# Kernel optimization log

Measured on AMD Instinct MI355X. Metric: run time of the kernel, lower is better.

The kernel has to match this reference:

```python
import jax, jax.numpy as jnp
import numpy as np

EMBED = 1024
HEADS = 16
HEAD_DIM = EMBED // HEADS
DIVIDER = int(np.sqrt(HEAD_DIM))  # torch code uses int(sqrt(head_dim)) == 8


def setup_inputs() -> dict:
    key = jax.random.key(0)
    ks = jax.random.split(key, 9)
    B, S = 2, 2048
    scale = 1.0 / np.sqrt(EMBED)
    def lin(kw, kb):
        W = jax.random.uniform(kw, (EMBED, EMBED), jnp.float32, -scale, scale)
        b = jax.random.uniform(kb, (EMBED,), jnp.float32, -scale, scale)
        return W, b
    Wq, bq = lin(ks[0], ks[1])
    Wk, bk = lin(ks[2], ks[3])
    Wv, bv = lin(ks[4], ks[5])
    Wo, bo = lin(ks[6], ks[7])
    x = jax.random.normal(ks[8], (B, S, EMBED), jnp.float32)
    return {"x": x, "Wq": Wq, "bq": bq, "Wk": Wk, "bk": bk,
            "Wv": Wv, "bv": bv, "Wo": Wo, "bo": bo}


def reference(x, Wq, bq, Wk, bk, Wv, bv, Wo, bo):
    B, S, _ = x.shape
    # projections (torch Linear: x @ W.T + b)
    q = x @ Wq.T + bq
    k = x @ Wk.T + bk
    v = x @ Wv.T + bv
    # split heads: [B, S, H, D] -> [B, H, S, D]
    def heads(t):
        return t.reshape(B, S, HEADS, HEAD_DIM).transpose(0, 2, 1, 3)
    q, k, v = heads(q), heads(k), heads(v)
    # scores [B, H, S, S]
    scores = jnp.einsum('bhsd,bhtd->bhst', q, k) / DIVIDER
    attn = jax.nn.softmax(scores, axis=-1)
    out = jnp.einsum('bhst,bhtd->bhsd', attn, v)
    out = out.transpose(0, 2, 1, 3).reshape(B, S, EMBED)
    return out @ Wo.T + bo
```

## Files before the change

kernel.cpp:

```cpp
#include <hip/hip_runtime.h>
#include <hip/hip_bf16.h>
#include <stdint.h>

using bf16 = __hip_bfloat16;
typedef __attribute__((ext_vector_type(8))) short   short8;
typedef __attribute__((ext_vector_type(4))) float   floatx4;
typedef __attribute__((ext_vector_type(2))) unsigned int uint2v;

static __device__ __forceinline__ unsigned short f2bf(float f) {
    return __builtin_bit_cast(unsigned short, __float2bfloat16(f));
}

static __device__ __forceinline__ uint4 load8bf(const void* p, size_t e, int f) {
    if (!f) return *(const uint4*)((const ushort*)p + e);
    const float* fp = (const float*)p + e;
    float4 a = *(const float4*)fp;
    float4 b = *(const float4*)(fp + 4);
    union { uint4 u; unsigned short s[8]; } r;
    r.s[0] = f2bf(a.x); r.s[1] = f2bf(a.y); r.s[2] = f2bf(a.z); r.s[3] = f2bf(a.w);
    r.s[4] = f2bf(b.x); r.s[5] = f2bf(b.y); r.s[6] = f2bf(b.z); r.s[7] = f2bf(b.w);
    return r.u;
}
static __device__ __forceinline__ float loadScalar(const void* p, int i, int f) {
    return f ? ((const float*)p)[i] : __bfloat162float(((const bf16*)p)[i]);
}

__global__ void detect_dtype(const ushort* __restrict__ x, int* __restrict__ flag) {
    __shared__ int cnt;
    if (threadIdx.x == 0) cnt = 0;
    __syncthreads();
    unsigned short u = x[threadIdx.x * 2];
    int e = (u >> 7) & 0xFF;
    int bad = (e > 133 || e < 94) ? 1 : 0;
    atomicAdd(&cnt, bad);
    __syncthreads();
    if (threadIdx.x == 0) *flag = (cnt > 64) ? 1 : 0;
}

template<int BM>
__global__ __launch_bounds__(512, 4)
void gemm_bt(const void* __restrict__ A,
             const void* __restrict__ Wa, const void* __restrict__ Wb,
             const void* __restrict__ Ba, const void* __restrict__ Bb,
             void* __restrict__ Oa, void* __restrict__ Ob_,
             int pa, int pb, int a_ext, int out_ext,
             const int* __restrict__ flagp)
{
    constexpr int MB = BM / 128;
    constexpr int P  = BM / 64;
    constexpr int SG = BM / 8;
    __shared__ ushort pool[BM * 64 + 4096];

    const int f  = *flagp;
    const int fA = a_ext ? f : 0;
    const int z  = blockIdx.z;
    const void* W   = z ? Wb : Wa;
    const void* Bi  = z ? Bb : Ba;
    void*       Out = z ? Ob_ : Oa;
    const int   pm  = z ? pb : pa;

    const int m0 = blockIdx.x * BM;
    const int n0 = blockIdx.y * 64;
    const int tid  = threadIdx.x;
    const int lane = tid & 63;
    const int wave = tid >> 6;
    const int r15  = lane & 15;
    const int quad = lane >> 4;

    const int srow = tid >> 3;
    const int sg   = tid & 7;

    ushort* xs  = pool;
    ushort* wsm = pool + BM * 64;

    floatx4 acc[MB][4];
#pragma unroll
    for (int mb = 0; mb < MB; mb++)
#pragma unroll
        for (int db = 0; db < 4; db++) acc[mb][db] = (floatx4){0.f, 0.f, 0.f, 0.f};

    uint4 apre[P], wpre;
#pragma unroll
    for (int p = 0; p < P; p++)
        apre[p] = load8bf(A, (size_t)(m0 + srow + p * 64) * 1024 + sg * 8, fA);
    wpre = load8bf(W, (size_t)(n0 + srow) * 1024 + sg * 8, f);

    for (int kb = 0; kb < 1024; kb += 64) {
#pragma unroll
        for (int p = 0; p < P; p++) {
            int row = srow + p * 64;
            *(uint4*)(&xs[row * 64 + ((sg ^ (row & 7)) << 3)]) = apre[p];
        }
        *(uint4*)(&wsm[srow * 64 + ((sg ^ (srow & 7)) << 3)]) = wpre;
        __syncthreads();
        if (kb + 64 < 1024) {
#pragma unroll
            for (int p = 0; p < P; p++)
                apre[p] = load8bf(A, (size_t)(m0 + srow + p * 64) * 1024
                                      + kb + 64 + sg * 8, fA);
            wpre = load8bf(W, (size_t)(n0 + srow) * 1024 + kb + 64 + sg * 8, f);
        }
#pragma unroll
        for (int ks = 0; ks < 2; ks++) {
            short8 af[MB];
#pragma unroll
            for (int mb = 0; mb < MB; mb++) {
                int arow = wave * (16 * MB) + mb * 16 + r15;
                af[mb] = *(const short8*)(
                    &xs[arow * 64 + (((ks * 4 + quad) ^ (arow & 7)) << 3)]);
            }
#pragma unroll
            for (int db = 0; db < 4; db++) {
                int brow = db * 16 + r15;
                short8 bv = *(const short8*)(
                    &wsm[brow * 64 + (((ks * 4 + quad) ^ (brow & 7)) << 3)]);
#pragma unroll
                for (int mb = 0; mb < MB; mb++)
                    acc[mb][db] = __builtin_amdgcn_mfma_f32_16x16x32_bf16(
                        af[mb], bv, acc[mb][db], 0, 0, 0);
            }
        }
        __syncthreads();
    }

    if (pm == 2) {
#pragma unroll
        for (int mb = 0; mb < MB; mb++)
#pragma unroll
            for (int db = 0; db < 4; db++) {
                int d = db * 16 + r15;
                float bias = loadScalar(Bi, n0 + d, f);
                int s4 = wave * (16 * MB) + mb * 16 + quad * 4;
                union { uint2 u; ushort us[4]; } pk;
#pragma unroll
                for (int r = 0; r < 4; r++) pk.us[r] = f2bf(acc[mb][db][r] + bias);
                *(uint2*)(&pool[d * BM + (((s4 >> 3) ^ (d & 15)) << 3) + (s4 & 7)])
                    = pk.u;
            }
        __syncthreads();
        const int b_  = m0 >> 11;
        const int h   = n0 >> 6;
        const int sl0 = m0 & 2047;
#pragma unroll
        for (int rr = 0; rr < (64 * SG) / 512; rr++) {
            int idx = rr * 512 + tid;
            int d = idx / SG, sgrp = idx % SG;
            uint4 v = *(const uint4*)(&pool[d * BM + ((sgrp ^ (d & 15)) << 3)]);
            *(uint4*)((ushort*)Out +
                      ((size_t)((b_ * 16 + h) * 64 + d) << 11) + sl0 + sgrp * 8) = v;
        }
        return;
    }

#pragma unroll
    for (int mb = 0; mb < MB; mb++)
#pragma unroll
        for (int db = 0; db < 4; db++) {
            int col = n0 + db * 16 + r15;
            float bias = loadScalar(Bi, col, f);
#pragma unroll
            for (int r = 0; r < 4; r++) {
                int row = m0 + wave * (16 * MB) + mb * 16 + quad * 4 + r;
                float v = acc[mb][db][r] + bias;
                if (pm == 1) {
                    int hh = col >> 6, d = col & 63;
                    int b_ = row >> 11, s = row & 2047;
                    ((ushort*)Out)[(((size_t)(b_ * 16 + hh) * 2048 + s) << 6) + d]
                        = f2bf(v);
                } else if (out_ext && f) {
                    ((float*)Out)[(size_t)row * 1024 + col] = v;
                } else {
                    ((ushort*)Out)[(size_t)row * 1024 + col] = f2bf(v);
                }
            }
        }
}

__global__ __launch_bounds__(512, 4)
void attn_fused(const void* __restrict__ x, const void* __restrict__ Wq,
                const void* __restrict__ bq,
                const ushort* __restrict__ K, const ushort* __restrict__ VT,
                ushort* __restrict__ AO, const int* __restrict__ flagp)
{
    __shared__ ushort pool[24576];

    const int f   = *flagp;
    const int bh  = blockIdx.x;
    const int h   = bh & 15, b_ = bh >> 4;
    const int q0  = blockIdx.y * 128;
    const int tid  = threadIdx.x;
    const int lane = tid & 63;
    const int wave = tid >> 6;
    const int qg   = wave >> 1;
    const int kh   = wave & 1;
    const int r15  = lane & 15;
    const int quad = lane >> 4;
    const size_t base = (size_t)bh << 17;

    const int srow = tid >> 3;
    const int sg   = tid & 7;

    uint4 kpre = *(const uint4*)(K  + base + (size_t)srow * 64   + sg * 8);
    uint4 vpre = *(const uint4*)(VT + base + (size_t)srow * 2048 + sg * 8);

    floatx4 qacc[4];
#pragma unroll
    for (int db = 0; db < 4; db++) qacc[db] = (floatx4){0.f,0.f,0.f,0.f};

    uint4 xpre[2], wpre;
#pragma unroll
    for (int p = 0; p < 2; p++)
        xpre[p] = load8bf(x, (size_t)(b_ * 2048 + q0 + srow + p * 64) * 1024
                              + sg * 8, f);
    wpre = load8bf(Wq, (size_t)(h * 64 + srow) * 1024 + sg * 8, f);

    for (int kb = 0; kb < 1024; kb += 64) {
        int buf = (kb >> 6) & 1;
        ushort* xs  = pool + buf * 8192;
        ushort* wsm = pool + 16384 + buf * 4096;
#pragma unroll
        for (int p = 0; p < 2; p++) {
            int row = srow + p * 64;
            *(uint4*)(&xs[row * 64 + ((sg ^ (row & 7)) << 3)]) = xpre[p];
        }
        *(uint4*)(&wsm[srow * 64 + ((sg ^ (srow & 7)) << 3)]) = wpre;
        __syncthreads();
        if (kb + 64 < 1024) {
#pragma unroll
            for (int p = 0; p < 2; p++)
                xpre[p] = load8bf(x, (size_t)(b_ * 2048 + q0 + srow + p * 64) * 1024
                                      + kb + 64 + sg * 8, f);
            wpre = load8bf(Wq, (size_t)(h * 64 + srow) * 1024 + kb + 64 + sg * 8, f);
        }
#pragma unroll
        for (int ks = 0; ks < 2; ks++) {
            int arow = wave * 16 + r15;
            short8 af = *(const short8*)(
                &xs[arow * 64 + (((ks * 4 + quad) ^ (arow & 7)) << 3)]);
#pragma unroll
            for (int db = 0; db < 4; db++) {
                int brow = db * 16 + r15;
                short8 bv = *(const short8*)(
                    &wsm[brow * 64 + (((ks * 4 + quad) ^ (brow & 7)) << 3)]);
                qacc[db] = __builtin_amdgcn_mfma_f32_16x16x32_bf16(
                    af, bv, qacc[db], 0, 0, 0);
            }
        }
    }

    ushort* Qs = pool;
    const float csc = 0.1803368801f;
#pragma unroll
    for (int db = 0; db < 4; db++) {
        int d = db * 16 + r15;
        float bias = loadScalar(bq, h * 64 + d, f);
#pragma unroll
        for (int r = 0; r < 4; r++) {
            int q = wave * 16 + quad * 4 + r;
            Qs[q * 64 + (((d >> 3) ^ (q & 7)) << 3) + (d & 7)] =
                f2bf((qacc[db][r] + bias) * csc);
        }
    }
    __syncthreads();
    short8 qf2[2][2];
#pragma unroll
    for (int qb = 0; qb < 2; qb++)
#pragma unroll
        for (int ks = 0; ks < 2; ks++) {
            int arow = qg * 32 + qb * 16 + r15;
            qf2[qb][ks] = *(const short8*)(
                &Qs[arow * 64 + (((ks * 4 + quad) ^ (arow & 7)) << 3)]);
        }
    __syncthreads();

    floatx4 oacc[2][4], lacc[2];
#pragma unroll
    for (int qb = 0; qb < 2; qb++) {
#pragma unroll
        for (int db = 0; db < 4; db++) oacc[qb][db] = (floatx4){0.f,0.f,0.f,0.f};
        lacc[qb] = (floatx4){0.f,0.f,0.f,0.f};
    }
    short8 ones;
#pragma unroll
    for (int j = 0; j < 8; j++) ones[j] = (short)0x3F80;

    for (int t0 = 0; t0 < 2048; t0 += 64) {
        int buf = (t0 >> 6) & 1;
        ushort* Ks = pool + buf * 4096;
        ushort* Vt = pool + 8192 + buf * 4096;
        *(uint4*)(&Ks[srow * 64 + ((sg ^ (srow & 7)) << 3)]) = kpre;
        *(uint4*)(&Vt[srow * 64 + ((sg ^ (srow & 7)) << 3)]) = vpre;
        __syncthreads();
        if (t0 < 1984) {
            kpre = *(const uint4*)(K  + base + (size_t)(t0 + 64 + srow) * 64
                                       + sg * 8);
            vpre = *(const uint4*)(VT + base + (size_t)srow * 2048
                                       + t0 + 64 + sg * 8);
        }

        floatx4 s[2][2];
#pragma unroll
        for (int mb = 0; mb < 2; mb++)
#pragma unroll
            for (int qb = 0; qb < 2; qb++) s[mb][qb] = (floatx4){0.f,0.f,0.f,0.f};
#pragma unroll
        for (int ks = 0; ks < 2; ks++)
#pragma unroll
            for (int mb = 0; mb < 2; mb++) {
                int arow = kh * 32 + mb * 16 + r15;
                short8 kf = *(const short8*)(
                    &Ks[arow * 64 + (((ks * 4 + quad) ^ (arow & 7)) << 3)]);
#pragma unroll
                for (int qb = 0; qb < 2; qb++)
                    s[mb][qb] = __builtin_amdgcn_mfma_f32_16x16x32_bf16(
                        kf, qf2[qb][ks], s[mb][qb], 0, 0, 0);
            }

        uint Lr[2][2], Hr[2][2];
#pragma unroll
        for (int mb = 0; mb < 2; mb++)
#pragma unroll
            for (int qb = 0; qb < 2; qb++) {
                uint b0 = __builtin_bit_cast(uint, __builtin_amdgcn_exp2f(s[mb][qb][0]));
                uint b1 = __builtin_bit_cast(uint, __builtin_amdgcn_exp2f(s[mb][qb][1]));
                uint b2 = __builtin_bit_cast(uint, __builtin_amdgcn_exp2f(s[mb][qb][2]));
                uint b3 = __builtin_bit_cast(uint, __builtin_amdgcn_exp2f(s[mb][qb][3]));
                Lr[mb][qb] = (b1 & 0xFFFF0000u) | (b0 >> 16);
                Hr[mb][qb] = (b3 & 0xFFFF0000u) | (b2 >> 16);
            }
        short8 pf[2];
#pragma unroll
        for (int qb = 0; qb < 2; qb++) {
            uint2v tL = __builtin_amdgcn_permlane32_swap(
                Lr[0][qb], Lr[1][qb], false, false);
            uint2v uL = __builtin_amdgcn_permlane16_swap(
                tL[0], tL[1], false, false);
            uint2v tH = __builtin_amdgcn_permlane32_swap(
                Hr[0][qb], Hr[1][qb], false, false);
            uint2v uH = __builtin_amdgcn_permlane16_swap(
                tH[0], tH[1], false, false);
            union { uint u[4]; short8 s8; } pk;
            pk.u[0] = uL[0]; pk.u[1] = uH[0]; pk.u[2] = uL[1]; pk.u[3] = uH[1];
            pf[qb] = pk.s8;
        }

#pragma unroll
        for (int db = 0; db < 4; db++) {
            int brow = db * 16 + r15;
            short8 vf = *(const short8*)(
                &Vt[brow * 64 + (((kh * 4 + quad) ^ (brow & 7)) << 3)]);
#pragma unroll
            for (int qb = 0; qb < 2; qb++)
                oacc[qb][db] = __builtin_amdgcn_mfma_f32_16x16x32_bf16(
                    pf[qb], vf, oacc[qb][db], 0, 0, 0);
        }
#pragma unroll
        for (int qb = 0; qb < 2; qb++)
            lacc[qb] = __builtin_amdgcn_mfma_f32_16x16x32_bf16(
                pf[qb], ones, lacc[qb], 0, 0, 0);
    }

    __syncthreads();
    {
        char* rb = (char*)pool + qg * 10240 + lane * 16;
        if (kh) {
#pragma unroll
            for (int qb = 0; qb < 2; qb++) {
#pragma unroll
                for (int db = 0; db < 4; db++)
                    *(floatx4*)(rb + (qb * 4 + db) * 1024) = oacc[qb][db];
                *(floatx4*)(rb + (8 + qb) * 1024) = lacc[qb];
            }
        }
        __syncthreads();
        if (!kh) {
#pragma unroll
            for (int qb = 0; qb < 2; qb++) {
#pragma unroll
                for (int db = 0; db < 4; db++)
                    oacc[qb][db] += *(const floatx4*)(rb + (qb * 4 + db) * 1024);
                lacc[qb] += *(const floatx4*)(rb + (8 + qb) * 1024);
            }
            float inv[2][4];
#pragma unroll
            for (int qb = 0; qb < 2; qb++)
#pragma unroll
                for (int r = 0; r < 4; r++) inv[qb][r] = 1.f / lacc[qb][r];
#pragma unroll
            for (int qb = 0; qb < 2; qb++)
#pragma unroll
                for (int db = 0; db < 4; db++) {
                    int d = db * 16 + r15;
#pragma unroll
                    for (int r = 0; r < 4; r++) {
                        int qi = q0 + qg * 32 + qb * 16 + quad * 4 + r;
                        AO[((size_t)(b_ * 2048 + qi) << 10) + h * 64 + d] =
                            f2bf(oacc[qb][db][r] * inv[qb][r]);
                    }
                }
        }
    }
}

__global__ void copy_u4(const uint4* __restrict__ src, uint4* __restrict__ dst) {
    size_t i = (size_t)blockIdx.x * 256 + threadIdx.x;
    dst[i] = src[i];
}

extern "C" void kernel_launch(void* const* d_in, const int* in_sizes, int n_in,
                              void* d_out, int out_size, void* d_ws, size_t ws_size,
                              hipStream_t stream)
{
    const void* x  = d_in[0];
    const void* Wq = d_in[1];
    const void* bq = d_in[2];
    const void* Wk = d_in[3];
    const void* bk = d_in[4];
    const void* Wv = d_in[5];
    const void* bv = d_in[6];
    const void* Wo = d_in[7];
    const void* bo = d_in[8];

    const size_t TEN = (size_t)2 * 16 * 2048 * 64;
    int*    flagp = (int*)d_ws;
    ushort* Kw    = (ushort*)((char*)d_ws + 256);
    ushort* Vw    = Kw + TEN;
    const bool big_ws = ws_size >= 3 * TEN * sizeof(ushort) + 256;
    ushort* AOw   = big_ws ? (Vw + TEN) : (ushort*)d_out;
    ushort* Oin   = big_ws ? AOw : Kw;

    detect_dtype<<<1, 256, 0, stream>>>((const ushort*)x, flagp);

    gemm_bt<128><<<dim3(32, 16, 2), dim3(512), 0, stream>>>(
        x, Wk, Wv, bk, bv, Kw, Vw, 1, 2, 1,
        0, flagp);

    attn_fused<<<dim3(32, 16), dim3(512), 0, stream>>>(
        x, Wq, bq, Kw, Vw, AOw, flagp);

    if (!big_ws)
        copy_u4<<<dim3(2048), dim3(256), 0, stream>>>(
            (const uint4*)d_out, (uint4*)Oin);

    gemm_bt<128><<<dim3(32, 16, 1), dim3(512), 0, stream>>>(
        Oin, Wo, Wo, bo, bo, d_out, d_out, 0, 0, 0,
        1, flagp);
}
```

Measured before the change: 224.1 us.

## Pre-convert inputs to bf16 and use direct global-to-LDS loads in GEMMs

```diff
diff --git a/kernel.cpp b/kernel.cpp
--- a/kernel.cpp
+++ b/kernel.cpp
@@ -24,6 +24,11 @@
 static __device__ __forceinline__ float loadScalar(const void* p, int i, int f) {
     return f ? ((const float*)p)[i] : __bfloat162float(((const bf16*)p)[i]);
 }
+
+#define GLL16(g, l)                                                          \
+    __builtin_amdgcn_global_load_lds(                                        \
+        (const __attribute__((address_space(1))) void*)(g),                  \
+        (__attribute__((address_space(3))) void*)(l), 16, 0, 0)
 
 __global__ void detect_dtype(const ushort* __restrict__ x, int* __restrict__ flag) {
     __shared__ int cnt;
@@ -35,6 +40,136 @@
     atomicAdd(&cnt, bad);
     __syncthreads();
     if (threadIdx.x == 0) *flag = (cnt > 64) ? 1 : 0;
+}
+
+__global__ void cvt_bf16(const void* __restrict__ x,  const void* __restrict__ Wq,
+                         const void* __restrict__ Wk, const void* __restrict__ Wv,
+                         const void* __restrict__ Wo,
+                         ushort* __restrict__ out, const int* __restrict__ flagp)
+{
+    const int f = *flagp;
+    const size_t M1 = (size_t)1 << 20, M4 = (size_t)4 << 20;
+    size_t i = ((size_t)blockIdx.x * 256 + threadIdx.x) * 8;
+    const void* src; size_t off;
+    if (i < M4)            { src = x;  off = i; }
+    else if (i < M4 + M1)  { src = Wq; off = i - M4; }
+    else if (i < M4 + 2*M1){ src = Wk; off = i - (M4 + M1); }
+    else if (i < M4 + 3*M1){ src = Wv; off = i - (M4 + 2*M1); }
+    else                   { src = Wo; off = i - (M4 + 3*M1); }
+    *(uint4*)(out + i) = load8bf(src, off, f);
+}
+
+__global__ __launch_bounds__(512, 4)
+void gemm_lds(const ushort* __restrict__ A,
+              const ushort* __restrict__ Wa, const ushort* __restrict__ Wb2,
+              const void* __restrict__ Ba, const void* __restrict__ Bb,
+              void* __restrict__ Oa, void* __restrict__ Ob_,
+              int pa, int pb, int out_ext, const int* __restrict__ flagp)
+{
+    __shared__ ushort pool[12288];
+
+    const int f  = *flagp;
+    const int z  = blockIdx.z;
+    const ushort* W  = z ? Wb2 : Wa;
+    const void*  Bi  = z ? Bb : Ba;
+    void*        Out = z ? Ob_ : Oa;
+    const int    pm  = z ? pb : pa;
+
+    const int m0 = blockIdx.x * 128;
+    const int n0 = blockIdx.y * 64;
+    const int tid  = threadIdx.x;
+    const int lane = tid & 63;
+    const int wave = tid >> 6;
+    const int r15  = lane & 15;
+    const int quad = lane >> 4;
+
+    const int l8 = lane >> 3, s8 = lane & 7;
+    const int ar0 = wave * 16 + l8;
+    const int ar1 = wave * 16 + 8 + l8;
+    const int wr  = wave * 8 + l8;
+    const ushort* gA0 = A + (size_t)(m0 + ar0) * 1024 + ((s8 ^ (ar0 & 7)) << 3);
+    const ushort* gA1 = A + (size_t)(m0 + ar1) * 1024 + ((s8 ^ (ar1 & 7)) << 3);
+    const ushort* gW  = W + (size_t)(n0 + wr) * 1024 + ((s8 ^ (wr & 7)) << 3);
+    ushort* lA0 = pool + (size_t)wave * 1024;
+    ushort* lA1 = pool + (size_t)wave * 1024 + 512;
+    ushort* lW  = pool + 8192 + (size_t)wave * 512;
+
+    floatx4 acc[4];
+#pragma unroll
+    for (int db = 0; db < 4; db++) acc[db] = (floatx4){0.f, 0.f, 0.f, 0.f};
+
+    ushort* xs  = pool;
+    ushort* wsm = pool + 8192;
+
+    for (int kb = 0; kb < 1024; kb += 64) {
+        GLL16(gA0 + kb, lA0);
+        GLL16(gA1 + kb, lA1);
+        GLL16(gW  + kb, lW);
+        __syncthreads();
+#pragma unroll
+        for (int ks = 0; ks < 2; ks++) {
+            int arow = wave * 16 + r15;
+            short8 af = *(const short8*)(
+                &xs[arow * 64 + (((ks * 4 + quad) ^ (arow & 7)) << 3)]);
+#pragma unroll
+            for (int db = 0; db < 4; db++) {
+                int brow = db * 16 + r15;
+                short8 bv = *(const short8*)(
+                    &wsm[brow * 64 + (((ks * 4 + quad) ^ (brow & 7)) << 3)]);
+                acc[db] = __builtin_amdgcn_mfma_f32_16x16x32_bf16(
+                    af, bv, acc[db], 0, 0, 0);
+            }
+        }
+        __syncthreads();
+    }
+
+    if (pm == 2) {
+#pragma unroll
+        for (int db = 0; db < 4; db++) {
+            int d = db * 16 + r15;
+            float bias = loadScalar(Bi, n0 + d, f);
+            int s4 = wave * 16 + quad * 4;
+            union { uint2 u; ushort us[4]; } pk;
+#pragma unroll
+            for (int r = 0; r < 4; r++) pk.us[r] = f2bf(acc[db][r] + bias);
+            *(uint2*)(&pool[d * 128 + (((s4 >> 3) ^ (d & 15)) << 3) + (s4 & 7)])
+                = pk.u;
+        }
+        __syncthreads();
+        const int b_  = m0 >> 11;
+        const int h   = n0 >> 6;
+        const int sl0 = m0 & 2047;
+#pragma unroll
+        for (int rr = 0; rr < 2; rr++) {
+            int idx = rr * 512 + tid;
+            int d = idx >> 4, sgrp = idx & 15;
+            uint4 v = *(const uint4*)(&pool[d * 128 + ((sgrp ^ (d & 15)) << 3)]);
+            *(uint4*)((ushort*)Out +
+                      ((size_t)((b_ * 16 + h) * 64 + d) << 11) + sl0 + sgrp * 8) = v;
+        }
+        return;
+    }
+
+#pragma unroll
+    for (int db = 0; db < 4; db++) {
+        int col = n0 + db * 16 + r15;
+        float bias = loadScalar(Bi, col, f);
+#pragma unroll
+        for (int r = 0; r < 4; r++) {
+            int row = m0 + wave * 16 + quad * 4 + r;
+            float v = acc[db][r] + bias;
+            if (pm == 1) {
+                int hh = col >> 6, d = col & 63;
+                int b_ = row >> 11, s = row & 2047;
+                ((ushort*)Out)[(((size_t)(b_ * 16 + hh) * 2048 + s) << 6) + d]
+                    = f2bf(v);
+            } else if (out_ext && f) {
+                ((float*)Out)[(size_t)row * 1024 + col] = v;
+            } else {
+                ((ushort*)Out)[(size_t)row * 1024 + col] = f2bf(v);
+            }
+        }
+    }
 }
 
 template<int BM>
@@ -180,11 +315,13 @@
 void attn_fused(const void* __restrict__ x, const void* __restrict__ Wq,
                 const void* __restrict__ bq,
                 const ushort* __restrict__ K, const ushort* __restrict__ VT,
-                ushort* __restrict__ AO, const int* __restrict__ flagp)
+                ushort* __restrict__ AO, const int* __restrict__ flagp,
+                int xisbf)
 {
     __shared__ ushort pool[24576];
 
     const int f   = *flagp;
+    const int fx  = xisbf ? 0 : f;
     const int bh  = blockIdx.x;
     const int h   = bh & 15, b_ = bh >> 4;
     const int q0  = blockIdx.y * 128;
@@ -211,8 +348,8 @@
 #pragma unroll
     for (int p = 0; p < 2; p++)
         xpre[p] = load8bf(x, (size_t)(b_ * 2048 + q0 + srow + p * 64) * 1024
-                              + sg * 8, f);
-    wpre = load8bf(Wq, (size_t)(h * 64 + srow) * 1024 + sg * 8, f);
+                              + sg * 8, fx);
+    wpre = load8bf(Wq, (size_t)(h * 64 + srow) * 1024 + sg * 8, fx);
 
     for (int kb = 0; kb < 1024; kb += 64) {
         int buf = (kb >> 6) & 1;
@@ -229,8 +366,8 @@
 #pragma unroll
             for (int p = 0; p < 2; p++)
                 xpre[p] = load8bf(x, (size_t)(b_ * 2048 + q0 + srow + p * 64) * 1024
-                                      + kb + 64 + sg * 8, f);
-            wpre = load8bf(Wq, (size_t)(h * 64 + srow) * 1024 + kb + 64 + sg * 8, f);
+                                      + kb + 64 + sg * 8, fx);
+            wpre = load8bf(Wq, (size_t)(h * 64 + srow) * 1024 + kb + 64 + sg * 8, fx);
         }
 #pragma unroll
         for (int ks = 0; ks < 2; ks++) {
@@ -422,27 +559,57 @@
     const void* bo = d_in[8];
 
     const size_t TEN = (size_t)2 * 16 * 2048 * 64;
+    const size_t M1  = (size_t)1 << 20;
     int*    flagp = (int*)d_ws;
     ushort* Kw    = (ushort*)((char*)d_ws + 256);
     ushort* Vw    = Kw + TEN;
-    const bool big_ws = ws_size >= 3 * TEN * sizeof(ushort) + 256;
-    ushort* AOw   = big_ws ? (Vw + TEN) : (ushort*)d_out;
-    ushort* Oin   = big_ws ? AOw : Kw;
+
+    const size_t need_cvt = 256 + (2 * TEN + 8 * M1) * sizeof(ushort);
+    const size_t need_aow = need_cvt + TEN * sizeof(ushort);
 
     detect_dtype<<<1, 256, 0, stream>>>((const ushort*)x, flagp);
 
-    gemm_bt<128><<<dim3(32, 16, 2), dim3(512), 0, stream>>>(
-        x, Wk, Wv, bk, bv, Kw, Vw, 1, 2, 1,
-        0, flagp);
-
-    attn_fused<<<dim3(32, 16), dim3(512), 0, stream>>>(
-        x, Wq, bq, Kw, Vw, AOw, flagp);
-
-    if (!big_ws)
-        copy_u4<<<dim3(2048), dim3(256), 0, stream>>>(
-            (const uint4*)d_out, (uint4*)Oin);
-
-    gemm_bt<128><<<dim3(32, 16, 1), dim3(512), 0, stream>>>(
-        Oin, Wo, Wo, bo, bo, d_out, d_out, 0, 0, 0,
-        1, flagp);
-}
+    if (ws_size >= need_cvt) {
+        ushort* CV  = Vw + TEN;
+        ushort* xb  = CV;
+        ushort* wqb = CV + 4 * M1;
+        ushort* wkb = CV + 5 * M1;
+        ushort* wvb = CV + 6 * M1;
+        ushort* wob = CV + 7 * M1;
+        const bool aow_ws = ws_size >= need_aow;
+        ushort* AOw = aow_ws ? (CV + 8 * M1) : (ushort*)d_out;
+        ushort* Oin = aow_ws ? AOw : Kw;
+
+        cvt_bf16<<<dim3(4096), dim3(256), 0, stream>>>(
+            x, Wq, Wk, Wv, Wo, CV, flagp);
+
+        gemm_lds<<<dim3(32, 16, 2), dim3(512), 0, stream>>>(
+            xb, wkb, wvb, bk, bv, Kw, Vw, 1, 2,
+            0, flagp);
+
+        attn_fused<<<dim3(32, 16), dim3(512), 0, stream>>>(
+            xb, wqb, bq, Kw, Vw, AOw, flagp, 1);
+
+        if (!aow_ws)
+            copy_u4<<<dim3(2048), dim3(256), 0, stream>>>(
+                (const uint4*)d_out, (uint4*)Oin);
+
+        gemm_lds<<<dim3(32, 16, 1), dim3(512), 0, stream>>>(
+            Oin, wob, wob, bo, bo, d_out, d_out, 0, 0,
+            1, flagp);
+    } else {
+        const bool big_ws = ws_size >= 3 * TEN * sizeof(ushort) + 256;
+        ushort* AOw = big_ws ? (Vw + TEN) : (ushort*)d_out;
+        ushort* Oin = big_ws ? AOw : Kw;
+
+        gemm_bt<128><<<dim3(32, 16, 2), dim3(512), 0, stream>>>(
+            x, Wk, Wv, bk, bv, Kw, Vw, 1, 2, 1, 0, flagp);
+        attn_fused<<<dim3(32, 16), dim3(512), 0, stream>>>(
+            x, Wq, bq, Kw, Vw, AOw, flagp, 0);
+        if (!big_ws)
+            copy_u4<<<dim3(2048), dim3(256), 0, stream>>>(
+                (const uint4*)d_out, (uint4*)Oin);
+        gemm_bt<128><<<dim3(32, 16, 1), dim3(512), 0, stream>>>(
+            Oin, Wo, Wo, bo, bo, d_out, d_out, 0, 0, 0, 1, flagp);
+    }
+}
```

Result: faster. 199.5 us (-11.0%).
